# Kernel tuning notes

Measured on AMD Instinct MI355X. Metric: run time of the kernel, lower is better.

Reference implementation:

```python
import jax, jax.numpy as jnp
import numpy as np

D_MODEL = 1024
NUM_HEADS = 16
HEAD_DIM = D_MODEL // NUM_HEADS
D_FF = 4096
THETA = 10000.0
MAX_SEQ_LEN = 2048
EPS = 1e-5


def _init_linear(key, out_f, in_f):
    std = np.sqrt(2.0 / (out_f + in_f))
    w = jax.random.truncated_normal(key, -3.0, 3.0, (out_f, in_f), dtype=jnp.float32) * std
    return w


def setup_inputs() -> dict:
    key = jax.random.key(0)
    ks = jax.random.split(key, 9)
    x = jax.random.normal(ks[0], (4, 2048, D_MODEL), dtype=jnp.float32)
    return {
        "x": x,
        "wq": _init_linear(ks[1], D_MODEL, D_MODEL),
        "wk": _init_linear(ks[2], D_MODEL, D_MODEL),
        "wv": _init_linear(ks[3], D_MODEL, D_MODEL),
        "wo": _init_linear(ks[4], D_MODEL, D_MODEL),
        "ln1_w": jnp.ones((D_MODEL,), jnp.float32),
        "ln2_w": jnp.ones((D_MODEL,), jnp.float32),
        "up_w": _init_linear(ks[5], D_FF, D_MODEL),
        "gate_w": _init_linear(ks[6], D_FF, D_MODEL),
        "down_w": _init_linear(ks[7], D_MODEL, D_FF),
    }


def _rmsnorm(x, w):
    xf = x.astype(jnp.float32)
    inv_rms = jax.lax.rsqrt(jnp.mean(xf * xf, axis=-1, keepdims=True) + EPS)
    return (xf * inv_rms * w).astype(x.dtype)


def _rope_tables(seq_len):
    inv_freq = 1.0 / THETA ** (jnp.arange(0, HEAD_DIM, 2, dtype=jnp.float32) / HEAD_DIM)
    t = jnp.arange(seq_len, dtype=jnp.float32)
    freqs = jnp.outer(t, inv_freq)  # [s, hd/2]
    return jnp.cos(freqs), jnp.sin(freqs)


def _apply_rope(x, cos, sin):
    # x: [b, h, s, hd]; cos/sin: [s, hd/2] -> broadcast over b,h
    xe = x[..., 0::2]
    xo = x[..., 1::2]
    oe = xe * cos - xo * sin
    oo = xo * cos + xe * sin
    return jnp.stack((oe, oo), axis=-1).reshape(x.shape)


def reference(x, wq, wk, wv, wo, ln1_w, ln2_w, up_w, gate_w, down_w):
    b, s, d = x.shape
    h, hd = NUM_HEADS, HEAD_DIM

    # --- attention sublayer (pre-norm) ---
    xn = _rmsnorm(x, ln1_w)
    q = (xn @ wq.T).reshape(b, s, h, hd).transpose(0, 2, 1, 3)
    k = (xn @ wk.T).reshape(b, s, h, hd).transpose(0, 2, 1, 3)
    v = (xn @ wv.T).reshape(b, s, h, hd).transpose(0, 2, 1, 3)

    cos, sin = _rope_tables(s)
    q = _apply_rope(q, cos, sin)
    k = _apply_rope(k, cos, sin)

    scale = 1.0 / jnp.sqrt(jnp.float32(hd))
    logits = jnp.einsum("bhqd,bhkd->bhqk", q, k)
    causal = jnp.tril(jnp.ones((s, s), dtype=bool))
    logits = jnp.where(causal, logits, -jnp.inf)
    attn = jax.nn.softmax(logits * scale, axis=-1)
    ao = jnp.einsum("bhqk,bhkd->bhqd", attn, v)
    ao = ao.transpose(0, 2, 1, 3).reshape(b, s, d) @ wo.T
    x = x + ao

    # --- SwiGLU FFN sublayer (pre-norm) ---
    xn = _rmsnorm(x, ln2_w)
    up = xn @ up_w.T
    gate = xn @ gate_w.T
    ff = (up * jax.nn.sigmoid(up) * gate) @ down_w.T
    return x + ff
```

## Files before the change

### kernel.cpp

```cpp
#include <hip/hip_runtime.h>
#include <stdint.h>

#define SEQ   2048
#define NTOK  8192

typedef unsigned short u16;
typedef __bf16 bf16x8 __attribute__((ext_vector_type(8)));
typedef float  f32x4  __attribute__((ext_vector_type(4)));
typedef float  f32x16 __attribute__((ext_vector_type(16)));

__device__ __forceinline__ float b2f(u16 b) {
    union { unsigned u; float f; } v; v.u = ((unsigned)b) << 16; return v.f;
}
__device__ __forceinline__ u16 f2b(float f) {
    union { float f; unsigned u; } v; v.f = f;
    unsigned r = (v.u + 0x7fffu + ((v.u >> 16) & 1u)) >> 16;
    return (u16)r;
}
__device__ __forceinline__ u16 f2b_trunc(float f) {
    union { float f; unsigned u; } v; v.f = f;
    return (u16)(v.u >> 16);
}

__device__ __forceinline__ void gl_lds16(const void* g, void* l) {
    __builtin_amdgcn_global_load_lds(
        (const __attribute__((address_space(1))) void*)g,
        (__attribute__((address_space(3))) void*)l,
        16, 0, 0);
}

__global__ __launch_bounds__(256)
void cvt_all(const float* __restrict__ wq, const float* __restrict__ wk,
             const float* __restrict__ wv, const float* __restrict__ wo,
             const float* __restrict__ wup, const float* __restrict__ wgt,
             const float* __restrict__ wdn,
             u16* __restrict__ dq, u16* __restrict__ dk, u16* __restrict__ dv,
             u16* __restrict__ dw, u16* __restrict__ dmu, u16* __restrict__ dd)
{
    const int bid = blockIdx.x;
    const float* s; u16* d; int osrc, odst;
    if (bid < 4096) {
        const int which = bid >> 10;
        osrc = odst = (bid & 1023) * 256 + threadIdx.x;
        s = which == 0 ? wq : which == 1 ? wk : which == 2 ? wv : wo;
        d = which == 0 ? dq : which == 1 ? dk : which == 2 ? dv : dw;
    } else {
        const int which = (bid - 4096) >> 12;
        const int o = ((bid - 4096) & 4095) * 256 + threadIdx.x;
        osrc = o;
        if (which == 2) { s = wdn; d = dd; odst = o; }
        else {
            s = which == 0 ? wup : wgt;
            d = dmu;
            const int row = o >> 8;
            const int rowp = ((row >> 4) << 5) + (row & 15) + (which == 0 ? 16 : 0);
            odst = rowp * 256 + (o & 255);
        }
    }
    float4 v = ((const float4*)s)[osrc];
    ushort4 ov;
    ov.x = f2b(v.x); ov.y = f2b(v.y); ov.z = f2b(v.z); ov.w = f2b(v.w);
    ((ushort4*)d)[odst] = ov;
}

template<int EPI>
__global__ __launch_bounds__(256)
void gemm_bt(const u16* __restrict__ A, const u16* __restrict__ B,
             void* __restrict__ C, const void* __restrict__ E,
             int M, int N, int K, int ldc, int coff)
{
    __shared__ __align__(16) u16 As[128 * 64];
    __shared__ __align__(16) u16 Bs[128 * 64];

    const int tid  = threadIdx.x;
    const int lane = tid & 63;
    const int wid  = tid >> 6;
    const int m0 = blockIdx.y * 128;
    const int n0 = blockIdx.x * 128;
    const int wm = (wid >> 1) * 64;
    const int wn = (wid & 1) * 64;
    const int l31 = lane & 31, kg = lane >> 5;

    f32x16 acc[2][2];
#pragma unroll
    for (int i = 0; i < 2; i++)
#pragma unroll
        for (int j = 0; j < 2; j++)
#pragma unroll
            for (int r = 0; r < 16; r++) acc[i][j][r] = 0.f;

    const u16* Ag[4]; const u16* Bg[4]; u16* Al[4]; u16* Bl[4];
#pragma unroll
    for (int j = 0; j < 4; j++) {
        const int q = j * 256 + tid;
        const int r = q >> 3, s = q & 7, c = s ^ (r & 7);
        Ag[j] = A + (size_t)(m0 + r) * K + c * 8;
        Bg[j] = B + (size_t)(n0 + r) * K + c * 8;
        Al[j] = As + q * 8;
        Bl[j] = Bs + q * 8;
    }

    int arow[2], brow[2];
#pragma unroll
    for (int i = 0; i < 2; i++) { arow[i] = wm + i * 32 + l31; }
#pragma unroll
    for (int j = 0; j < 2; j++) { brow[j] = wn + j * 32 + l31; }

    for (int kt = 0; kt < K; kt += 64) {
        __syncthreads();
#pragma unroll
        for (int j = 0; j < 4; j++) {
            gl_lds16(Ag[j] + kt, Al[j]);
            gl_lds16(Bg[j] + kt, Bl[j]);
        }
        __syncthreads();

#pragma unroll
        for (int s = 0; s < 4; s++) {
            const int ch = s * 2 + kg;
            bf16x8 af[2], bf[2];
#pragma unroll
            for (int i = 0; i < 2; i++)
                af[i] = *(const bf16x8*)(
                    &As[arow[i] * 64 + ((ch ^ (arow[i] & 7)) * 8)]);
#pragma unroll
            for (int j = 0; j < 2; j++)
                bf[j] = *(const bf16x8*)(
                    &Bs[brow[j] * 64 + ((ch ^ (brow[j] & 7)) * 8)]);
#pragma unroll
            for (int i = 0; i < 2; i++)
#pragma unroll
                for (int j = 0; j < 2; j++)
                    acc[i][j] = __builtin_amdgcn_mfma_f32_32x32x16_bf16(
                        af[i], bf[j], acc[i][j], 0, 0, 0);
        }
    }

#pragma unroll
    for (int i = 0; i < 2; i++) {
#pragma unroll
        for (int r = 0; r < 16; r++) {
            const int row = m0 + wm + i * 32 + (r & 3) + 8 * (r >> 2) + 4 * kg;
#pragma unroll
            for (int j = 0; j < 2; j++) {
                const int col = n0 + wn + j * 32 + l31;
                const size_t idx = (size_t)row * ldc + coff + col;
                const float v = acc[i][j][r];
                if (EPI == 0) {
                    ((u16*)C)[idx] = f2b(v);
                } else {
                    ((float*)C)[idx] = v + ((const float*)E)[idx];
                }
            }
        }
    }
}

#define MIDBAR \
    __builtin_amdgcn_s_barrier(); \
    asm volatile("s_waitcnt lgkmcnt(0)" ::: "memory"); \
    __builtin_amdgcn_sched_barrier(0);

#define PBAR \
    __builtin_amdgcn_s_barrier(); \
    asm volatile("" ::: "memory"); \
    __builtin_amdgcn_sched_barrier(0);

#define VMBAR4 \
    asm volatile("s_waitcnt vmcnt(4)" ::: "memory"); \
    __builtin_amdgcn_s_barrier(); \
    asm volatile("" ::: "memory"); \
    __builtin_amdgcn_sched_barrier(0);

#define VMBAR0 \
    asm volatile("s_waitcnt vmcnt(0)" ::: "memory"); \
    __builtin_amdgcn_s_barrier(); \
    asm volatile("" ::: "memory"); \
    __builtin_amdgcn_sched_barrier(0);

#define LDA(bufi, mh) { \
    const u16* _ab = Ab##bufi + (mh) * 4096; \
    _Pragma("unroll") \
    for (int _m = 0; _m < 4; ++_m) { \
        Aq[_m][0] = *(const bf16x8*)(_ab + _m * 1024 + axor0); \
        Aq[_m][1] = *(const bf16x8*)(_ab + _m * 1024 + axor1); \
    } }

#define LDB(bufi, nh) { \
    const u16* _bb = Bb##bufi + (nh) * 2048; \
    _Pragma("unroll") \
    for (int _n = 0; _n < 2; ++_n) { \
        Bq[nh][_n][0] = *(const bf16x8*)(_bb + _n * 1024 + axor0); \
        Bq[nh][_n][1] = *(const bf16x8*)(_bb + _n * 1024 + axor1); \
    } }

#define MM(mh, nh) \
    __builtin_amdgcn_s_setprio(1); \
    { _Pragma("unroll") \
      for (int _m = 0; _m < 4; ++_m) { \
        _Pragma("unroll") \
        for (int _n = 0; _n < 2; ++_n) { \
            acc[(mh)*4+_m][(nh)*2+_n] = __builtin_amdgcn_mfma_f32_16x16x32_bf16( \
                Aq[_m][0], Bq[nh][_n][0], acc[(mh)*4+_m][(nh)*2+_n], 0, 0, 0); \
            acc[(mh)*4+_m][(nh)*2+_n] = __builtin_amdgcn_mfma_f32_16x16x32_bf16( \
                Aq[_m][1], Bq[nh][_n][1], acc[(mh)*4+_m][(nh)*2+_n], 0, 0, 0); \
        } } } \
    __builtin_amdgcn_s_setprio(0);

#define STAGE_A(tile, half) { \
    const u16* _s = pA0 + (size_t)(half) * 131072 + (size_t)(tile) * 64; \
    u16* _d = lA0 + ((tile) & 1) * 16384 + (half) * 8192; \
    gl_lds16(_s, _d); \
    gl_lds16(_s + 65536, _d + 4096); }

#define STAGE_B(tile, half) { \
    const u16* _s = pB0 + (size_t)(half) * 131072 + (size_t)(tile) * 64; \
    u16* _d = lB0 + ((tile) & 1) * 16384 + (half) * 8192; \
    gl_lds16(_s, _d); \
    gl_lds16(_s + 65536, _d + 4096); }

__global__ __launch_bounds__(512, 2)
void gemm8_mlp(const u16* __restrict__ A, const u16* __restrict__ Bc,
               u16* __restrict__ H)
{
    __shared__ __align__(16) u16 As[32768];
    __shared__ __align__(16) u16 Bs[32768];

    const int tid = threadIdx.x, lane = tid & 63, wid = tid >> 6;
    const int wr = wid >> 2, wc = wid & 3;
    const int r15 = lane & 15, ks = lane >> 4;
    const int m0 = blockIdx.y * 256, n0 = blockIdx.x * 256;

    const int axor0 = ((ks) ^ (r15 & 7)) * 8;
    const int axor1 = ((4 + ks) ^ (r15 & 7)) * 8;
    const u16* Ab0 = As + wr * 8192 + r15 * 64;
    const u16* Ab1 = As + 16384 + wr * 8192 + r15 * 64;
    const u16* Bb0 = Bs + (wc >> 1) * 8192 + (wc & 1) * 4096 + r15 * 64;
    const u16* Bb1 = Bs + 16384 + (wc >> 1) * 8192 + (wc & 1) * 4096 + r15 * 64;

    const int r0 = tid >> 3, c0 = (tid & 7) ^ (r0 & 7);
    const u16* pA0 = A  + (size_t)(m0 + r0) * 1024 + c0 * 8;
    const u16* pB0 = Bc + (size_t)(n0 + r0) * 1024 + c0 * 8;
    u16* lA0 = As + tid * 8;
    u16* lB0 = Bs + tid * 8;

    f32x4 acc[8][4];
#pragma unroll
    for (int m = 0; m < 8; ++m)
#pragma unroll
        for (int n = 0; n < 4; ++n)
            acc[m][n] = (f32x4){0.f, 0.f, 0.f, 0.f};

    bf16x8 Aq[4][2], Bq[2][2][2];

    STAGE_A(0, 0); STAGE_A(0, 1);
    STAGE_B(0, 0); STAGE_B(0, 1);
    STAGE_B(1, 0); STAGE_B(1, 1);
    asm volatile("s_waitcnt vmcnt(4)" ::: "memory");
    __builtin_amdgcn_s_barrier();
    asm volatile("" ::: "memory");
    __builtin_amdgcn_sched_barrier(0);

    for (int i = 0; i < 8; ++i) {
        const int t1 = 2 * i + 1;
        const int t2 = 2 * i + 2;
        const int t3 = 2 * i + 3;
        const bool st = (i < 7);

        LDA(0, 0); LDB(0, 0);
        STAGE_A(t1, 0);
        MIDBAR; MM(0, 0); PBAR;
        LDB(0, 1);
        STAGE_A(t1, 1);
        MIDBAR; MM(0, 1); PBAR;
        LDA(0, 1);
        if (st) STAGE_B(t2, 0);
        MIDBAR; MM(1, 1); PBAR;
        if (st) STAGE_B(t2, 1);
        MIDBAR; MM(1, 0);
        if (i == 7) { VMBAR0; } else { VMBAR4; }

        LDA(1, 0); LDB(1, 0);
        if (st) STAGE_A(t2, 0);
        MIDBAR; MM(0, 0); PBAR;
        LDB(1, 1);
        if (st) STAGE_A(t2, 1);
        MIDBAR; MM(0, 1); PBAR;
        LDA(1, 1);
        if (st) STAGE_B(t3, 0);
        MIDBAR; MM(1, 1); PBAR;
        if (st) STAGE_B(t3, 1);
        MIDBAR; MM(1, 0);
        VMBAR4;
    }

    const int orow0 = m0 + wr * 128;
    const int ocol0 = (n0 >> 1) + wc * 32;
#pragma unroll
    for (int m = 0; m < 8; ++m) {
#pragma unroll
        for (int p = 0; p < 2; ++p) {
#pragma unroll
            for (int r = 0; r < 4; ++r) {
                const int row = orow0 + m * 16 + ks * 4 + r;
                const int col = ocol0 + p * 16 + r15;
                const float g = acc[m][2 * p][r];
                const float u = acc[m][2 * p + 1][r];
                H[(size_t)row * 4096 + col] = f2b(u / (1.f + __expf(-u)) * g);
            }
        }
    }
}

__global__ __launch_bounds__(256)
void rmsnorm_k(const float* __restrict__ xin, const float* __restrict__ w,
               u16* __restrict__ o)
{
    const int t = blockIdx.x;
    const int tid = threadIdx.x;
    float4 xv = ((const float4*)xin)[(size_t)t * 256 + tid];
    float ss = xv.x * xv.x + xv.y * xv.y + xv.z * xv.z + xv.w * xv.w;
#pragma unroll
    for (int off = 32; off > 0; off >>= 1) ss += __shfl_down(ss, off);
    __shared__ float red[4];
    const int lane = tid & 63, wv_ = tid >> 6;
    if (lane == 0) red[wv_] = ss;
    __syncthreads();
    const float tot = red[0] + red[1] + red[2] + red[3];
    const float inv = rsqrtf(tot * (1.f / 1024.f) + 1e-5f);
    float4 ww = ((const float4*)w)[tid];
    ushort4 ov;
    ov.x = f2b(xv.x * inv * ww.x);
    ov.y = f2b(xv.y * inv * ww.y);
    ov.z = f2b(xv.z * inv * ww.z);
    ov.w = f2b(xv.w * inv * ww.w);
    ((ushort4*)o)[(size_t)t * 256 + tid] = ov;
}

#define QSCALE 0.18033688011112042f

__global__ void rope_tab(float* __restrict__ cs, float* __restrict__ sn)
{
    const int s = blockIdx.x;
    const int i = threadIdx.x;
    const double inv = exp(-((double)(2 * i) / 64.0) * log(10000.0));
    const double ang = (double)s * inv;
    cs[s * 32 + i] = (float)cos(ang);
    sn[s * 32 + i] = (float)sin(ang);
}

__global__ __launch_bounds__(256)
void rope_apply(u16* __restrict__ qkv, const float* __restrict__ cs,
                const float* __restrict__ sn)
{
    const int t = blockIdx.x;
    const int s = t & (SEQ - 1);
    u16* row = qkv + (size_t)t * 3072;
    __shared__ float c_s[32], s_s[32];
    if (threadIdx.x < 32) {
        c_s[threadIdx.x] = cs[s * 32 + threadIdx.x];
        s_s[threadIdx.x] = sn[s * 32 + threadIdx.x];
    }
    __syncthreads();
#pragma unroll
    for (int rr = 0; rr < 2; rr++) {
        const int item = rr * 256 + threadIdx.x;
        const int hh = item >> 5, i = item & 31;
        const int f = hh * 64 + 2 * i;
        const float c = c_s[i], sv = s_s[i];
        float xe = b2f(row[f]), xo = b2f(row[f + 1]);
        row[f]     = f2b((xe * c - xo * sv) * QSCALE);
        row[f + 1] = f2b((xo * c + xe * sv) * QSCALE);
        xe = b2f(row[1024 + f]); xo = b2f(row[1024 + f + 1]);
        row[1024 + f]     = f2b(xe * c - xo * sv);
        row[1024 + f + 1] = f2b(xo * c + xe * sv);
    }
}

__global__ __launch_bounds__(256)
void vtrans(const u16* __restrict__ qkv, u16* __restrict__ vt)
{
    __shared__ u16 Ld[64 * 264];
    const int bh = blockIdx.x, st = blockIdx.y;
    const int b = bh >> 4, h = bh & 15;
    const int tid = threadIdx.x;
    const u16* src = qkv + ((size_t)(b * SEQ + st * 256 + tid)) * 3072 + 2048 + h * 64;
    uint4 v[8];
#pragma unroll
    for (int c = 0; c < 8; c++) v[c] = *(const uint4*)(src + c * 8);
#pragma unroll
    for (int c = 0; c < 8; c++) {
        const u16* pv = (const u16*)&v[c];
#pragma unroll
        for (int j = 0; j < 8; j++)
            Ld[(c * 8 + j) * 264 + tid] = pv[j];
    }
    __syncthreads();
    u16* dst = vt + (size_t)bh * (64 * SEQ) + st * 256;
#pragma unroll
    for (int cc = 0; cc < 8; cc++) {
        const int c = cc * 256 + tid;
        const int d = c >> 5, t8 = (c & 31) * 8;
        *(uint4*)(dst + (size_t)d * SEQ + t8) = *(const uint4*)(&Ld[d * 264 + t8]);
    }
}

__global__ __launch_bounds__(512)
void attn(const u16* __restrict__ qkv, const u16* __restrict__ vt,
          u16* __restrict__ ao)
{
    __shared__ __align__(16) u16 Ks[64 * 72];
    __shared__ __align__(16) u16 Vt[64 * 72];
    __shared__ __align__(16) u16 Ps[8][16 * 72];

    const int bh = blockIdx.x;
    const int qy = blockIdx.y;
    const int b = bh >> 4, h = bh & 15;
    const int tid = threadIdx.x, lane = tid & 63, wid = tid >> 6;
    const int am = lane & 15, grp = lane >> 4;
    const size_t tok0 = (size_t)b * SEQ;
    const u16* qbase = qkv + tok0 * 3072 + h * 64;
    const u16* kbase = qbase + 1024;
    const u16* vtg = vt + (size_t)bh * (64 * SEQ);

    union { uint4 u; bf16x8 b; } onesu;
    onesu.u = (uint4){0x3f803f80u, 0x3f803f80u, 0x3f803f80u, 0x3f803f80u};
    const bf16x8 ones = onesu.b;

    const int srow = tid >> 3, sc8 = (tid & 7) * 8;

#pragma unroll
    for (int tile = 0; tile < 2; tile++) {
        const int yt = tile == 0 ? qy : 15 - qy;
        const int qrow0 = yt * 128 + wid * 16;

        bf16x8 qf[2];
        {
            const u16* qp = qbase + (size_t)(qrow0 + am) * 3072 + grp * 8;
            qf[0] = *(const bf16x8*)(qp);
            qf[1] = *(const bf16x8*)(qp + 32);
        }

        f32x4 O[4], Ol;
#pragma unroll
        for (int j = 0; j < 4; j++) O[j] = (f32x4){0.f, 0.f, 0.f, 0.f};
        Ol = (f32x4){0.f, 0.f, 0.f, 0.f};

        const int ktend = yt * 128 + 64;
        for (int kt = 0; kt <= ktend; kt += 64) {
            __syncthreads();
            *(uint4*)(&Ks[srow * 72 + sc8]) =
                *(const uint4*)(kbase + (size_t)(kt + srow) * 3072 + sc8);
            *(uint4*)(&Vt[srow * 72 + sc8]) =
                *(const uint4*)(vtg + (size_t)srow * SEQ + kt + sc8);
            __syncthreads();

            if (kt > qrow0 + 15) continue;

            f32x4 st[4];
#pragma unroll
            for (int kk = 0; kk < 4; kk++) {
                const u16* kb = &Ks[(kk * 16 + am) * 72 + grp * 8];
                bf16x8 k0 = *(const bf16x8*)(kb);
                bf16x8 k1 = *(const bf16x8*)(kb + 32);
                f32x4 s = (f32x4){0.f, 0.f, 0.f, 0.f};
                s = __builtin_amdgcn_mfma_f32_16x16x32_bf16(qf[0], k0, s, 0, 0, 0);
                s = __builtin_amdgcn_mfma_f32_16x16x32_bf16(qf[1], k1, s, 0, 0, 0);
                st[kk] = s;
            }
            if (kt + 63 > qrow0) {
#pragma unroll
                for (int kk = 0; kk < 4; kk++) {
                    const int kg2 = kt + kk * 16 + am;
#pragma unroll
                    for (int r = 0; r < 4; r++) {
                        const int qg = qrow0 + grp * 4 + r;
                        if (kg2 > qg) st[kk][r] = -1e30f;
                    }
                }
            }
#pragma unroll
            for (int kk = 0; kk < 4; kk++)
#pragma unroll
                for (int r = 0; r < 4; r++)
                    st[kk][r] = exp2f(st[kk][r]);

            u16* pw = &Ps[wid][0];
#pragma unroll
            for (int kk = 0; kk < 4; kk++)
#pragma unroll
                for (int r = 0; r < 4; r++)
                    pw[(grp * 4 + r) * 72 + kk * 16 + am] = f2b_trunc(st[kk][r]);
            asm volatile("s_waitcnt lgkmcnt(0)" ::: "memory");

#pragma unroll
            for (int hh = 0; hh < 2; hh++) {
                bf16x8 pf = *(const bf16x8*)(&pw[am * 72 + hh * 32 + grp * 8]);
                Ol = __builtin_amdgcn_mfma_f32_16x16x32_bf16(pf, ones, Ol, 0, 0, 0);
#pragma unroll
                for (int jt = 0; jt < 4; jt++) {
                    bf16x8 vf = *(const bf16x8*)(
                        &Vt[(jt * 16 + am) * 72 + hh * 32 + grp * 8]);
                    O[jt] = __builtin_amdgcn_mfma_f32_16x16x32_bf16(
                        pf, vf, O[jt], 0, 0, 0);
                }
            }
        }

        u16* aorow = ao + (tok0 + qrow0) * 1024 + h * 64;
#pragma unroll
        for (int r = 0; r < 4; r++) {
            const int q = grp * 4 + r;
            const float invl = 1.f / Ol[r];
#pragma unroll
            for (int jt = 0; jt < 4; jt++)
                aorow[(size_t)q * 1024 + jt * 16 + am] = f2b(O[jt][r] * invl);
        }
    }
}

extern "C" void kernel_launch(void* const* d_in, const int* in_sizes, int n_in,
                              void* d_out, int out_size, void* d_ws, size_t ws_size,
                              hipStream_t stream)
{
    (void)in_sizes; (void)n_in; (void)out_size; (void)ws_size;
    const float* x     = (const float*)d_in[0];
    const float* wq    = (const float*)d_in[1];
    const float* wk    = (const float*)d_in[2];
    const float* wv    = (const float*)d_in[3];
    const float* wo    = (const float*)d_in[4];
    const float* ln1   = (const float*)d_in[5];
    const float* ln2   = (const float*)d_in[6];
    const float* wup   = (const float*)d_in[7];
    const float* wgate = (const float*)d_in[8];
    const float* wdown = (const float*)d_in[9];
    float* out = (float*)d_out;
    char* ws = (char*)d_ws;
    const size_t MB = 1024 * 1024;

    u16*   xn   = (u16*)(ws);
    u16*   ao   = (u16*)(ws);
    u16*   qkv  = (u16*)(ws + 16 * MB);
    u16*   hbuf = (u16*)(ws + 16 * MB);
    u16*   vtb  = (u16*)(ws + 64 * MB);
    float* x1   = (float*)(ws + 80 * MB);
    u16*   bwq  = (u16*)(ws + 112 * MB);
    u16*   bwk  = (u16*)(ws + 114 * MB);
    u16*   bwv  = (u16*)(ws + 116 * MB);
    u16*   bwo  = (u16*)(ws + 118 * MB);
    u16*   bwmu = (u16*)(ws + 120 * MB);
    u16*   bwdn = (u16*)(ws + 136 * MB);
    float* cst  = (float*)(ws + 144 * MB);
    float* snt  = (float*)(ws + 144 * MB + 262144);

    cvt_all<<<16384, 256, 0, stream>>>(wq, wk, wv, wo, wup, wgate, wdown,
                                       bwq, bwk, bwv, bwo, bwmu, bwdn);

    rope_tab<<<SEQ, 32, 0, stream>>>(cst, snt);
    rmsnorm_k<<<NTOK, 256, 0, stream>>>(x, ln1, xn);
    gemm_bt<0><<<dim3(24, 64), 256, 0, stream>>>(xn, bwq, qkv, nullptr, NTOK, 3072, 1024, 3072, 0);
    rope_apply<<<NTOK, 256, 0, stream>>>(qkv, cst, snt);
    vtrans<<<dim3(64, 8), 256, 0, stream>>>(qkv, vtb);
    attn<<<dim3(64, 8), 512, 0, stream>>>(qkv, vtb, ao);
    gemm_bt<1><<<dim3(8, 64), 256, 0, stream>>>(ao, bwo, x1, x, NTOK, 1024, 1024, 1024, 0);
    rmsnorm_k<<<NTOK, 256, 0, stream>>>(x1, ln2, xn);
    gemm8_mlp<<<dim3(32, 32), 512, 0, stream>>>(xn, bwmu, hbuf);
    gemm_bt<1><<<dim3(8, 64), 256, 0, stream>>>(hbuf, bwdn, out, x1, NTOK, 1024, 4096, 1024, 0);
}
```

Before: 565.8 us.

## Add 8-wave pipelined GEMM kernel for FFN down projection with fused residual

Replaces the generic gemm_bt call for the down projection (K=4096) with a dedicated 512-thread kernel using 256x128 tiles, double-buffered direct global-to-LDS staging, swizzled LDS reads, and interleaved barriers with setprio around the MFMA bursts, modeled on the existing MLP kernel. It also merges the two vmcnt barrier macros into one parameterized macro. The aim is better MFMA utilization and load/compute overlap on the long-K GEMM. The cost is fewer blocks (256) on a large GPU and a hand-tuned pipeline whose correctness depends on the precise wait counts.

```diff
diff --git a/kernel.cpp b/kernel.cpp
--- a/kernel.cpp
+++ b/kernel.cpp
@@ -166,14 +166,8 @@
     asm volatile("" ::: "memory"); \
     __builtin_amdgcn_sched_barrier(0);
 
-#define VMBAR4 \
-    asm volatile("s_waitcnt vmcnt(4)" ::: "memory"); \
-    __builtin_amdgcn_s_barrier(); \
-    asm volatile("" ::: "memory"); \
-    __builtin_amdgcn_sched_barrier(0);
-
-#define VMBAR0 \
-    asm volatile("s_waitcnt vmcnt(0)" ::: "memory"); \
+#define VMBARN(n) \
+    asm volatile("s_waitcnt vmcnt(" #n ")" ::: "memory"); \
     __builtin_amdgcn_s_barrier(); \
     asm volatile("" ::: "memory"); \
     __builtin_amdgcn_sched_barrier(0);
@@ -278,7 +272,7 @@
         MIDBAR; MM(1, 1); PBAR;
         if (st) STAGE_B(t2, 1);
         MIDBAR; MM(1, 0);
-        if (i == 7) { VMBAR0; } else { VMBAR4; }
+        if (i == 7) { VMBARN(0); } else { VMBARN(4); }
 
         LDA(1, 0); LDB(1, 0);
         if (st) STAGE_A(t2, 0);
@@ -291,7 +285,7 @@
         MIDBAR; MM(1, 1); PBAR;
         if (st) STAGE_B(t3, 1);
         MIDBAR; MM(1, 0);
-        VMBAR4;
+        VMBARN(4);
     }
 
     const int orow0 = m0 + wr * 128;
@@ -307,6 +301,138 @@
                 const float g = acc[m][2 * p][r];
                 const float u = acc[m][2 * p + 1][r];
                 H[(size_t)row * 4096 + col] = f2b(u / (1.f + __expf(-u)) * g);
+            }
+        }
+    }
+}
+
+#define DLDA(bufi, mh) { \
+    const u16* _ab = dAb##bufi + (mh) * 2048; \
+    _Pragma("unroll") \
+    for (int _m = 0; _m < 2; ++_m) { \
+        Aq[_m][0] = *(const bf16x8*)(_ab + _m * 1024 + axor0); \
+        Aq[_m][1] = *(const bf16x8*)(_ab + _m * 1024 + axor1); \
+    } }
+
+#define DLDB(bufi, nh) { \
+    const u16* _bb = dBb##bufi + (nh) * 2048; \
+    _Pragma("unroll") \
+    for (int _n = 0; _n < 2; ++_n) { \
+        Bq[nh][_n][0] = *(const bf16x8*)(_bb + _n * 1024 + axor0); \
+        Bq[nh][_n][1] = *(const bf16x8*)(_bb + _n * 1024 + axor1); \
+    } }
+
+#define DMM(mh, nh) \
+    __builtin_amdgcn_s_setprio(1); \
+    { _Pragma("unroll") \
+      for (int _m = 0; _m < 2; ++_m) { \
+        _Pragma("unroll") \
+        for (int _n = 0; _n < 2; ++_n) { \
+            acc[(mh)*2+_m][(nh)*2+_n] = __builtin_amdgcn_mfma_f32_16x16x32_bf16( \
+                Aq[_m][0], Bq[nh][_n][0], acc[(mh)*2+_m][(nh)*2+_n], 0, 0, 0); \
+            acc[(mh)*2+_m][(nh)*2+_n] = __builtin_amdgcn_mfma_f32_16x16x32_bf16( \
+                Aq[_m][1], Bq[nh][_n][1], acc[(mh)*2+_m][(nh)*2+_n], 0, 0, 0); \
+        } } } \
+    __builtin_amdgcn_s_setprio(0);
+
+#define DSTAGE_A(tile, half) { \
+    const u16* _s = dpA + (size_t)(half) * 524288 + (size_t)(tile) * 64; \
+    u16* _d = dlA + ((tile) & 1) * 16384 + (half) * 8192; \
+    gl_lds16(_s, _d); \
+    gl_lds16(_s + 262144, _d + 4096); }
+
+#define DSTAGE_B(tile, half) { \
+    const u16* _s = dpB + (size_t)(half) * 262144 + (size_t)(tile) * 64; \
+    u16* _d = dlB + ((tile) & 1) * 8192 + (half) * 4096; \
+    gl_lds16(_s, _d); }
+
+__global__ __launch_bounds__(512, 2)
+void gemm8_dn(const u16* __restrict__ A, const u16* __restrict__ B,
+              float* __restrict__ C, const float* __restrict__ E)
+{
+    __shared__ __align__(16) u16 As[32768];
+    __shared__ __align__(16) u16 Bs[16384];
+
+    const int tid = threadIdx.x, lane = tid & 63, wid = tid >> 6;
+    const int wr = wid >> 1, wc = wid & 1;
+    const int r15 = lane & 15, ks = lane >> 4;
+    const int m0 = blockIdx.y * 256, n0 = blockIdx.x * 128;
+
+    const int axor0 = ((ks) ^ (r15 & 7)) * 8;
+    const int axor1 = ((4 + ks) ^ (r15 & 7)) * 8;
+    const u16* dAb0 = As + (wr * 64 + r15) * 64;
+    const u16* dAb1 = As + 16384 + (wr * 64 + r15) * 64;
+    const u16* dBb0 = Bs + (wc * 64 + r15) * 64;
+    const u16* dBb1 = Bs + 8192 + (wc * 64 + r15) * 64;
+
+    const int r0 = tid >> 3, c0 = (tid & 7) ^ (r0 & 7);
+    const u16* dpA = A + (size_t)(m0 + r0) * 4096 + c0 * 8;
+    const u16* dpB = B + (size_t)(n0 + r0) * 4096 + c0 * 8;
+    u16* dlA = As + tid * 8;
+    u16* dlB = Bs + tid * 8;
+
+    f32x4 acc[4][4];
+#pragma unroll
+    for (int m = 0; m < 4; ++m)
+#pragma unroll
+        for (int n = 0; n < 4; ++n)
+            acc[m][n] = (f32x4){0.f, 0.f, 0.f, 0.f};
+
+    bf16x8 Aq[2][2], Bq[2][2][2];
+
+    DSTAGE_A(0, 0); DSTAGE_A(0, 1);
+    DSTAGE_B(0, 0); DSTAGE_B(0, 1);
+    DSTAGE_B(1, 0); DSTAGE_B(1, 1);
+    asm volatile("s_waitcnt vmcnt(2)" ::: "memory");
+    __builtin_amdgcn_s_barrier();
+    asm volatile("" ::: "memory");
+    __builtin_amdgcn_sched_barrier(0);
+
+    for (int i = 0; i < 32; ++i) {
+        const int t1 = 2 * i + 1;
+        const int t2 = 2 * i + 2;
+        const int t3 = 2 * i + 3;
+        const bool st = (i < 31);
+
+        DLDA(0, 0); DLDB(0, 0);
+        DSTAGE_A(t1, 0);
+        MIDBAR; DMM(0, 0); PBAR;
+        DLDB(0, 1);
+        DSTAGE_A(t1, 1);
+        MIDBAR; DMM(0, 1); PBAR;
+        DLDA(0, 1);
+        if (st) DSTAGE_B(t2, 0);
+        MIDBAR; DMM(1, 1); PBAR;
+        if (st) DSTAGE_B(t2, 1);
+        MIDBAR; DMM(1, 0);
+        if (i == 31) { VMBARN(0); } else { VMBARN(2); }
+
+        DLDA(1, 0); DLDB(1, 0);
+        if (st) DSTAGE_A(t2, 0);
+        MIDBAR; DMM(0, 0); PBAR;
+        DLDB(1, 1);
+        if (st) DSTAGE_A(t2, 1);
+        MIDBAR; DMM(0, 1); PBAR;
+        DLDA(1, 1);
+        if (st) DSTAGE_B(t3, 0);
+        MIDBAR; DMM(1, 1); PBAR;
+        if (st) DSTAGE_B(t3, 1);
+        MIDBAR; DMM(1, 0);
+        VMBARN(2);
+    }
+
+    const int orow0 = m0 + wr * 64;
+    const int ocol0 = n0 + wc * 64;
+#pragma unroll
+    for (int m = 0; m < 4; ++m) {
+#pragma unroll
+        for (int n = 0; n < 4; ++n) {
+#pragma unroll
+            for (int r = 0; r < 4; ++r) {
+                const int row = orow0 + m * 16 + ks * 4 + r;
+                const int col = ocol0 + n * 16 + r15;
+                const size_t idx = (size_t)row * 1024 + col;
+                C[idx] = acc[m][n][r] + E[idx];
             }
         }
     }
@@ -565,5 +691,5 @@
     gemm_bt<1><<<dim3(8, 64), 256, 0, stream>>>(ao, bwo, x1, x, NTOK, 1024, 1024, 1024, 0);
     rmsnorm_k<<<NTOK, 256, 0, stream>>>(x1, ln2, xn);
     gemm8_mlp<<<dim3(32, 32), 512, 0, stream>>>(xn, bwmu, hbuf);
-    gemm_bt<1><<<dim3(8, 64), 256, 0, stream>>>(hbuf, bwdn, out, x1, NTOK, 1024, 4096, 1024, 0);
-}
+    gemm8_dn<<<dim3(8, 32), 512, 0, stream>>>(hbuf, bwdn, out, x1);
+}
```

Result: slower. 583.2 us (+3.1%).

## Double-buffer attention K/V tiles with direct global-to-LDS loads and XOR swizzle

Applied to the files above, without the earlier changes.

The attention kernel now double-buffers its K and V shared-memory tiles. It prefetches the next 64-key tile with direct global-to-LDS loads while the current tile is computed, and uses a single barrier per iteration instead of two syncthreads. The padded 72-wide LDS layout is replaced by an XOR-swizzled 64-wide layout to avoid bank conflicts without padding. The GEMM wait macros are merged into one parameterised macro with no behaviour change. This doubles the K/V LDS footprint and relies on gl_lds16 being correct for the swizzled destinations.

```diff
diff --git a/kernel.cpp b/kernel.cpp
--- a/kernel.cpp
+++ b/kernel.cpp
@@ -166,14 +166,8 @@
     asm volatile("" ::: "memory"); \
     __builtin_amdgcn_sched_barrier(0);
 
-#define VMBAR4 \
-    asm volatile("s_waitcnt vmcnt(4)" ::: "memory"); \
-    __builtin_amdgcn_s_barrier(); \
-    asm volatile("" ::: "memory"); \
-    __builtin_amdgcn_sched_barrier(0);
-
-#define VMBAR0 \
-    asm volatile("s_waitcnt vmcnt(0)" ::: "memory"); \
+#define VMBARN(n) \
+    asm volatile("s_waitcnt vmcnt(" #n ")" ::: "memory"); \
     __builtin_amdgcn_s_barrier(); \
     asm volatile("" ::: "memory"); \
     __builtin_amdgcn_sched_barrier(0);
@@ -278,7 +272,7 @@
         MIDBAR; MM(1, 1); PBAR;
         if (st) STAGE_B(t2, 1);
         MIDBAR; MM(1, 0);
-        if (i == 7) { VMBAR0; } else { VMBAR4; }
+        if (i == 7) { VMBARN(0); } else { VMBARN(4); }
 
         LDA(1, 0); LDB(1, 0);
         if (st) STAGE_A(t2, 0);
@@ -291,7 +285,7 @@
         MIDBAR; MM(1, 1); PBAR;
         if (st) STAGE_B(t3, 1);
         MIDBAR; MM(1, 0);
-        VMBAR4;
+        VMBARN(4);
     }
 
     const int orow0 = m0 + wr * 128;
@@ -409,8 +403,8 @@
 void attn(const u16* __restrict__ qkv, const u16* __restrict__ vt,
           u16* __restrict__ ao)
 {
-    __shared__ __align__(16) u16 Ks[64 * 72];
-    __shared__ __align__(16) u16 Vt[64 * 72];
+    __shared__ __align__(16) u16 Ks[2][64 * 64];
+    __shared__ __align__(16) u16 Vs[2][64 * 64];
     __shared__ __align__(16) u16 Ps[8][16 * 72];
 
     const int bh = blockIdx.x;
@@ -427,7 +421,12 @@
     onesu.u = (uint4){0x3f803f80u, 0x3f803f80u, 0x3f803f80u, 0x3f803f80u};
     const bf16x8 ones = onesu.b;
 
-    const int srow = tid >> 3, sc8 = (tid & 7) * 8;
+    const int srow = tid >> 3;
+    const int scsw = ((tid & 7) ^ (srow & 7)) * 8;
+    const u16* ksrc = kbase + (size_t)srow * 3072 + scsw;
+    const u16* vsrc = vtg + (size_t)srow * SEQ + scsw;
+    u16* kdst[2] = { &Ks[0][tid * 8], &Ks[1][tid * 8] };
+    u16* vdst[2] = { &Vs[0][tid * 8], &Vs[1][tid * 8] };
 
 #pragma unroll
     for (int tile = 0; tile < 2; tile++) {
@@ -447,64 +446,83 @@
         Ol = (f32x4){0.f, 0.f, 0.f, 0.f};
 
         const int ktend = yt * 128 + 64;
+
+        gl_lds16(ksrc, kdst[0]);
+        gl_lds16(vsrc, vdst[0]);
+        asm volatile("s_waitcnt vmcnt(0)" ::: "memory");
+        __builtin_amdgcn_s_barrier();
+        asm volatile("" ::: "memory");
+        __builtin_amdgcn_sched_barrier(0);
+
+        int buf = 0;
         for (int kt = 0; kt <= ktend; kt += 64) {
-            __syncthreads();
-            *(uint4*)(&Ks[srow * 72 + sc8]) =
-                *(const uint4*)(kbase + (size_t)(kt + srow) * 3072 + sc8);
-            *(uint4*)(&Vt[srow * 72 + sc8]) =
-                *(const uint4*)(vtg + (size_t)srow * SEQ + kt + sc8);
-            __syncthreads();
-
-            if (kt > qrow0 + 15) continue;
-
-            f32x4 st[4];
-#pragma unroll
-            for (int kk = 0; kk < 4; kk++) {
-                const u16* kb = &Ks[(kk * 16 + am) * 72 + grp * 8];
-                bf16x8 k0 = *(const bf16x8*)(kb);
-                bf16x8 k1 = *(const bf16x8*)(kb + 32);
-                f32x4 s = (f32x4){0.f, 0.f, 0.f, 0.f};
-                s = __builtin_amdgcn_mfma_f32_16x16x32_bf16(qf[0], k0, s, 0, 0, 0);
-                s = __builtin_amdgcn_mfma_f32_16x16x32_bf16(qf[1], k1, s, 0, 0, 0);
-                st[kk] = s;
+            if (kt + 64 <= ktend) {
+                gl_lds16(ksrc + (size_t)(kt + 64) * 3072, kdst[buf ^ 1]);
+                gl_lds16(vsrc + (kt + 64), vdst[buf ^ 1]);
             }
-            if (kt + 63 > qrow0) {
+
+            if (kt <= qrow0 + 15) {
+                const u16* kbuf = &Ks[0][0] + buf * 4096;
+                const u16* vbuf = &Vs[0][0] + buf * 4096;
+
+                f32x4 st[4];
 #pragma unroll
                 for (int kk = 0; kk < 4; kk++) {
-                    const int kg2 = kt + kk * 16 + am;
-#pragma unroll
-                    for (int r = 0; r < 4; r++) {
-                        const int qg = qrow0 + grp * 4 + r;
-                        if (kg2 > qg) st[kk][r] = -1e30f;
+                    const int rk = kk * 16 + am;
+                    bf16x8 k0 = *(const bf16x8*)(
+                        &kbuf[rk * 64 + ((grp ^ (rk & 7)) * 8)]);
+                    bf16x8 k1 = *(const bf16x8*)(
+                        &kbuf[rk * 64 + (((grp + 4) ^ (rk & 7)) * 8)]);
+                    f32x4 s = (f32x4){0.f, 0.f, 0.f, 0.f};
+                    s = __builtin_amdgcn_mfma_f32_16x16x32_bf16(qf[0], k0, s, 0, 0, 0);
+                    s = __builtin_amdgcn_mfma_f32_16x16x32_bf16(qf[1], k1, s, 0, 0, 0);
+                    st[kk] = s;
+                }
+                if (kt + 63 > qrow0) {
+#pragma unroll
+                    for (int kk = 0; kk < 4; kk++) {
+                        const int kg2 = kt + kk * 16 + am;
+#pragma unroll
+                        for (int r = 0; r < 4; r++) {
+                            const int qg = qrow0 + grp * 4 + r;
+                            if (kg2 > qg) st[kk][r] = -1e30f;
+                        }
+                    }
+                }
+#pragma unroll
+                for (int kk = 0; kk < 4; kk++)
+#pragma unroll
+                    for (int r = 0; r < 4; r++)
+                        st[kk][r] = exp2f(st[kk][r]);
+
+                u16* pw = &Ps[wid][0];
+#pragma unroll
+                for (int kk = 0; kk < 4; kk++)
+#pragma unroll
+                    for (int r = 0; r < 4; r++)
+                        pw[(grp * 4 + r) * 72 + kk * 16 + am] = f2b_trunc(st[kk][r]);
+                asm volatile("s_waitcnt lgkmcnt(0)" ::: "memory");
+
+#pragma unroll
+                for (int hh = 0; hh < 2; hh++) {
+                    bf16x8 pf = *(const bf16x8*)(&pw[am * 72 + hh * 32 + grp * 8]);
+                    Ol = __builtin_amdgcn_mfma_f32_16x16x32_bf16(pf, ones, Ol, 0, 0, 0);
+#pragma unroll
+                    for (int jt = 0; jt < 4; jt++) {
+                        const int rv = jt * 16 + am;
+                        bf16x8 vf = *(const bf16x8*)(
+                            &vbuf[rv * 64 + (((hh * 4 + grp) ^ (rv & 7)) * 8)]);
+                        O[jt] = __builtin_amdgcn_mfma_f32_16x16x32_bf16(
+                            pf, vf, O[jt], 0, 0, 0);
                     }
                 }
             }
-#pragma unroll
-            for (int kk = 0; kk < 4; kk++)
-#pragma unroll
-                for (int r = 0; r < 4; r++)
-                    st[kk][r] = exp2f(st[kk][r]);
-
-            u16* pw = &Ps[wid][0];
-#pragma unroll
-            for (int kk = 0; kk < 4; kk++)
-#pragma unroll
-                for (int r = 0; r < 4; r++)
-                    pw[(grp * 4 + r) * 72 + kk * 16 + am] = f2b_trunc(st[kk][r]);
-            asm volatile("s_waitcnt lgkmcnt(0)" ::: "memory");
-
-#pragma unroll
-            for (int hh = 0; hh < 2; hh++) {
-                bf16x8 pf = *(const bf16x8*)(&pw[am * 72 + hh * 32 + grp * 8]);
-                Ol = __builtin_amdgcn_mfma_f32_16x16x32_bf16(pf, ones, Ol, 0, 0, 0);
-#pragma unroll
-                for (int jt = 0; jt < 4; jt++) {
-                    bf16x8 vf = *(const bf16x8*)(
-                        &Vt[(jt * 16 + am) * 72 + hh * 32 + grp * 8]);
-                    O[jt] = __builtin_amdgcn_mfma_f32_16x16x32_bf16(
-                        pf, vf, O[jt], 0, 0, 0);
-                }
-            }
+
+            asm volatile("s_waitcnt vmcnt(0)" ::: "memory");
+            __builtin_amdgcn_s_barrier();
+            asm volatile("" ::: "memory");
+            __builtin_amdgcn_sched_barrier(0);
+            buf ^= 1;
         }
 
         u16* aorow = ao + (tok0 + qrow0) * 1024 + h * 64;
```

Measured after the change: 587.1 us. +3.8%, slower.
